# Kernel optimization log

Measured on AMD Instinct MI355X. Metric: run time of the kernel, lower is better.

## Reference

```python
import math
import jax, jax.numpy as jnp
import numpy as np

DIM = 256
B, S = 4, 4096

def setup_inputs() -> dict:
    key = jax.random.key(0)
    k1, k2, k3, k4 = jax.random.split(key, 4)
    x = jax.random.normal(k1, (B, S, DIM), dtype=jnp.float32)
    W = jax.random.normal(k2, (3 * DIM, DIM), dtype=jnp.float32) * 0.02
    b = jax.random.normal(k3, (3 * DIM,), dtype=jnp.float32) * 0.02
    attention_mask = jax.random.randint(k4, (B, 1, S), 0, 2, dtype=jnp.int32)
    return {"x": x, "W": W, "b": b, "attention_mask": attention_mask}

def reference(x, W, b, attention_mask):
    # qkv projection: Linear(dim, 3*dim) -> x @ W^T + b
    qkv = jnp.einsum("bsd,ed->bse", x, W) + b  # [B,S,3*DIM]
    q, k, v = jnp.split(qkv, 3, axis=-1)
    # NOTE: module computes q @ v^T (not q @ k^T) -- faithful to source
    scores = jnp.einsum("bqd,bkd->bqk", q, v) / math.sqrt(DIM)  # [B,S,S]
    scores = jnp.where(attention_mask == 0, -jnp.inf, scores)
    attn = jax.nn.softmax(scores, axis=-1)
    # dropout in eval mode -> identity
    out = jnp.einsum("bqk,bkd->bqd", attn, v)  # [B,S,DIM]
    return out
```

## Files before the change

kernel.cpp:

```cpp
#include <hip/hip_runtime.h>
#include <hip/hip_bf16.h>

#define DIMC 256
#define NB 4
#define NS 4096
#define KT 64
#define VS_ELEMS (KT * DIMC)

typedef __attribute__((ext_vector_type(4))) float f32x4;
typedef __attribute__((ext_vector_type(8))) short bf16x8;

__device__ __forceinline__ ushort f2bf(float f) {
  __hip_bfloat16 h = __float2bfloat16(f);
  return *reinterpret_cast<ushort*>(&h);
}
__device__ __forceinline__ float bf2f(ushort h) {
  uint u = ((uint)h) << 16;
  float f;
  __builtin_memcpy(&f, &u, 4);
  return f;
}

__device__ __forceinline__ void gload16(const ushort* g, ushort* l) {
  __builtin_amdgcn_global_load_lds(
      (const __attribute__((address_space(1))) unsigned int*)g,
      (__attribute__((address_space(3))) unsigned int*)l,
      16, 0, 0);
}

__global__ __launch_bounds__(256) void prep_kernel(
    const float* __restrict__ W, const int* __restrict__ mask,
    ushort* __restrict__ Whl, uint* __restrict__ pm32)
{
  if (blockIdx.x < 512) {
    const int col = blockIdx.x;
    const int k = threadIdx.x;
    const int srcrow = (col < 256) ? col : (col + 256);
    float f = W[(size_t)srcrow * 256 + k];
    ushort h = f2bf(f);
    Whl[(size_t)col * 256 + k] = h;
    Whl[131072 + (size_t)col * 256 + k] = f2bf(f - bf2f(h));
  } else {
    int t = (blockIdx.x - 512) * 256 + threadIdx.x;
    int b = t >> 7;
    int kt = (t >> 1) & 63;
    int kh = t & 1;
    const int* mrow = mask + b * NS + kt * 64 + kh * 32;
    uint wd = 0;
    for (int g = 0; g < 4; ++g)
      for (int ntl = 0; ntl < 2; ++ntl)
        for (int r = 0; r < 4; ++r)
          if (mrow[ntl * 16 + 4 * g + r] != 0) wd |= 1u << (8 * g + ntl * 4 + r);
    pm32[t] = wd;
  }
}

__global__ __launch_bounds__(256) void qv_proj_kernel(
    const float* __restrict__ x, const ushort* __restrict__ Whl,
    const float* __restrict__ bias,
    ushort* __restrict__ qb, ushort* __restrict__ vb, ushort* __restrict__ vtb)
{
  const int tid  = threadIdx.x;
  const int w    = tid >> 6;
  const int lane = tid & 63;
  const int l15  = lane & 15;
  const int g    = (lane >> 4) & 3;
  const int r0   = blockIdx.x << 6;
  const int colbase = w << 7;

  __shared__ ushort olds[64 * 520];

  f32x4 acc[4][8];
  #pragma unroll
  for (int rt = 0; rt < 4; ++rt)
    #pragma unroll
    for (int ct = 0; ct < 8; ++ct) { acc[rt][ct].x=0.f; acc[rt][ct].y=0.f; acc[rt][ct].z=0.f; acc[rt][ct].w=0.f; }

  #pragma unroll 1
  for (int st = 0; st < 8; ++st) {
    bf16x8 xh[4], xl[4];
    #pragma unroll
    for (int rt = 0; rt < 4; ++rt) {
      const float* p = x + (size_t)(r0 + rt * 16 + l15) * DIMC + st * 32 + g * 8;
      float4 f0 = *(const float4*)p;
      float4 f1 = *(const float4*)(p + 4);
      union { bf16x8 v; ushort u[8]; } uh, ul;
      #pragma unroll
      for (int e = 0; e < 8; ++e) {
        float fe = (e < 4) ? ((const float*)&f0)[e] : ((const float*)&f1)[e - 4];
        ushort h = f2bf(fe);
        uh.u[e] = h;
        ul.u[e] = f2bf(fe - bf2f(h));
      }
      xh[rt] = uh.v;
      xl[rt] = ul.v;
    }
    #pragma unroll
    for (int ct = 0; ct < 8; ++ct) {
      const ushort* wp = Whl + (size_t)(colbase + ct * 16 + l15) * 256 + st * 32 + g * 8;
      bf16x8 wh = *(const bf16x8*)wp;
      bf16x8 wl = *(const bf16x8*)(wp + 131072);
      #pragma unroll
      for (int rt = 0; rt < 4; ++rt) {
        acc[rt][ct] = __builtin_amdgcn_mfma_f32_16x16x32_bf16(xh[rt], wh, acc[rt][ct], 0, 0, 0);
        acc[rt][ct] = __builtin_amdgcn_mfma_f32_16x16x32_bf16(xl[rt], wh, acc[rt][ct], 0, 0, 0);
        acc[rt][ct] = __builtin_amdgcn_mfma_f32_16x16x32_bf16(xh[rt], wl, acc[rt][ct], 0, 0, 0);
      }
    }
  }

  const float qscale = (colbase < 256) ? 0.0625f : 1.0f;
  #pragma unroll
  for (int ct = 0; ct < 8; ++ct) {
    const int col = colbase + ct * 16 + l15;
    const float bv = bias[(col < 256) ? col : (col + 256)];
    #pragma unroll
    for (int rt = 0; rt < 4; ++rt) {
      #pragma unroll
      for (int r = 0; r < 4; ++r)
        olds[(rt * 16 + 4 * g + r) * 520 + col] = f2bf((acc[rt][ct][r] + bv) * qscale);
    }
  }
  __syncthreads();

  #pragma unroll
  for (int i = 0; i < 16; ++i) {
    int task = tid + i * 256;
    int row = task >> 6, ch = task & 63;
    uint4 d = *(const uint4*)&olds[row * 520 + ch * 8];
    if (ch < 32) *(uint4*)&qb[(size_t)(r0 + row) * DIMC + ch * 8] = d;
    else         *(uint4*)&vb[(size_t)(r0 + row) * DIMC + (ch - 32) * 8] = d;
  }
  const int bbp = r0 >> 12;
  const int s0  = r0 & (NS - 1);
  const int vcol = tid;
  #pragma unroll
  for (int o = 0; o < 8; ++o) {
    union { uint4 v; ushort u[8]; } pk;
    #pragma unroll
    for (int j = 0; j < 8; ++j)
      pk.u[j] = olds[(o * 8 + j) * 520 + 256 + vcol];
    *(uint4*)&vtb[((size_t)(bbp * DIMC + vcol)) * NS + s0 + o * 8] = pk.v;
  }
}

__global__ __launch_bounds__(512, 1) void attn_kernel(
    const ushort* __restrict__ qb, const ushort* __restrict__ vb,
    const ushort* __restrict__ vtb, const uint* __restrict__ pm32,
    float* __restrict__ outA, float* __restrict__ opB,
    float* __restrict__ mlA, float* __restrict__ mlB)
{
  const int tid  = threadIdx.x;
  const int w    = tid >> 6;
  const int lane = tid & 63;
  const int l15  = lane & 15;
  const int g    = (lane >> 4) & 3;
  const int kh   = w & 1;
  const int pq   = w >> 1;

  const int s     = blockIdx.x & 1;
  const int qb128 = blockIdx.x >> 1;
  const int qrow0 = qb128 << 7;
  const int bb    = qrow0 >> 12;
  const int koff  = s << 11;

  float* opart = s ? opB : outA;
  float* mlp   = s ? mlB : mlA;

  extern __shared__ __align__(16) char smem[];
  uint*   pmlds = (uint*)smem;
  ushort* vs0  = (ushort*)(smem + 1024);
  ushort* vs1  = vs0 + VS_ELEMS;
  ushort* vt0  = vs1 + VS_ELEMS;
  ushort* vt1  = vt0 + VS_ELEMS;
  ushort* psb  = vt1 + VS_ELEMS;

  bf16x8 qreg[2][8];
  #pragma unroll
  for (int qt = 0; qt < 2; ++qt) {
    const int qrow = qrow0 + (pq << 5) + (qt << 4) + l15;
    #pragma unroll
    for (int st = 0; st < 8; ++st)
      qreg[qt][st] = *(const bf16x8*)&qb[(size_t)qrow * DIMC + ((st * 4 + g) << 3)];
  }

  if (tid < 128) pmlds[tid] = pm32[(bb << 7) + tid];

  auto stage_vs = [&](int kt, ushort* vsN) {
    const ushort* vbase = vb + ((size_t)(bb * NS + koff + kt * KT)) * DIMC;
    #pragma unroll
    for (int i = 0; i < 4; ++i) {
      int rr0 = (w << 3) + (i << 1);
      int row = rr0 + (lane >> 5);
      int cs  = lane & 31;
      gload16(vbase + row * DIMC + ((cs ^ (row & 7)) << 3), vsN + (rr0 << 8));
    }
  };
  auto stage_vt = [&](int kt, ushort* vtN) {
    #pragma unroll
    for (int i = 0; i < 4; ++i) {
      int d0 = i << 6;
      int dim = (d0 + lane) ^ ((w & 3) << 1);
      gload16(vtb + ((size_t)(bb * DIMC + dim)) * NS + koff + kt * KT + (w << 3),
              vtN + ((w << 8) + d0) * 8);
    }
  };

  stage_vs(0, vs0);
  __syncthreads();

  f32x4 acc_o[2][8];
  #pragma unroll
  for (int qt = 0; qt < 2; ++qt)
    #pragma unroll
    for (int nt = 0; nt < 8; ++nt) { acc_o[qt][nt].x=0.f; acc_o[qt][nt].y=0.f; acc_o[qt][nt].z=0.f; acc_o[qt][nt].w=0.f; }
  float l_s[2] = {0.f, 0.f};

  ushort* psw = psb + pq * (32 * 72);

  #pragma unroll 1
  for (int t = 0; t < 32; ++t) {
    ushort* vsQ = (t & 1) ? vs1 : vs0;
    ushort* vsS = (t & 1) ? vs0 : vs1;
    ushort* vtS = (t & 1) ? vt1 : vt0;
    ushort* vtP = (t & 1) ? vt0 : vt1;

    if (t + 1 < 32) stage_vs(t + 1, vsS);
    stage_vt(t, vtS);

    f32x4 sacc[2][2];
    #pragma unroll
    for (int qt = 0; qt < 2; ++qt) {
      sacc[qt][0].x=0.f; sacc[qt][0].y=0.f; sacc[qt][0].z=0.f; sacc[qt][0].w=0.f;
      sacc[qt][1] = sacc[qt][0];
    }
    __builtin_amdgcn_s_setprio(1);
    #pragma unroll
    for (int st = 0; st < 8; ++st) {
      const int key0 = (kh << 5) + l15;
      bf16x8 af0 = *(const bf16x8*)&vsQ[(key0 * 32 + ((st * 4 + g) ^ (key0 & 7))) * 8];
      const int key1 = key0 + 16;
      bf16x8 af1 = *(const bf16x8*)&vsQ[(key1 * 32 + ((st * 4 + g) ^ (key1 & 7))) * 8];
      #pragma unroll
      for (int qt = 0; qt < 2; ++qt) {
        sacc[qt][0] = __builtin_amdgcn_mfma_f32_16x16x32_bf16(af0, qreg[qt][st], sacc[qt][0], 0, 0, 0);
        sacc[qt][1] = __builtin_amdgcn_mfma_f32_16x16x32_bf16(af1, qreg[qt][st], sacc[qt][1], 0, 0, 0);
      }
    }
    __builtin_amdgcn_s_setprio(0);

    if (t > 0) {
      bf16x8 pa[2][2];
      #pragma unroll
      for (int qt = 0; qt < 2; ++qt)
        #pragma unroll
        for (int ks2 = 0; ks2 < 2; ++ks2)
          pa[qt][ks2] = *(const bf16x8*)&psw[((qt << 4) + l15) * 72 + (ks2 << 5) + (g << 3)];
      __builtin_amdgcn_s_setprio(1);
      #pragma unroll
      for (int ntl = 0; ntl < 8; ++ntl) {
        const int d = ((kh << 3) + ntl) * 16 + l15;
        #pragma unroll
        for (int ks2 = 0; ks2 < 2; ++ks2) {
          const int kc = (ks2 << 2) + g;
          bf16x8 vf = *(const bf16x8*)&vtP[((kc << 8) + (d ^ ((kc & 3) << 1))) * 8];
          acc_o[0][ntl] = __builtin_amdgcn_mfma_f32_16x16x32_bf16(vf, pa[0][ks2], acc_o[0][ntl], 0, 0, 0);
          acc_o[1][ntl] = __builtin_amdgcn_mfma_f32_16x16x32_bf16(vf, pa[1][ks2], acc_o[1][ntl], 0, 0, 0);
        }
      }
      __builtin_amdgcn_s_setprio(0);
    }

    const int ktg = (s << 5) + t;
    uint mybits = (pmlds[(ktg << 1) + kh] >> (g << 3)) & 0xffu;
    float pv[2][8];
    #pragma unroll
    for (int qt = 0; qt < 2; ++qt) {
      #pragma unroll
      for (int ntl = 0; ntl < 2; ++ntl)
        #pragma unroll
        for (int r = 0; r < 4; ++r) {
          float vv = (mybits & (1u << (ntl * 4 + r))) ? sacc[qt][ntl][r] : -1e30f;
          pv[qt][ntl * 4 + r] = __expf(vv);
        }
      float rs = ((pv[qt][0] + pv[qt][1]) + (pv[qt][2] + pv[qt][3])) +
                 ((pv[qt][4] + pv[qt][5]) + (pv[qt][6] + pv[qt][7]));
      rs += __shfl_xor(rs, 16);
      rs += __shfl_xor(rs, 32);
      l_s[qt] += rs;
    }

    asm volatile("s_waitcnt lgkmcnt(0)" ::: "memory");
    __builtin_amdgcn_sched_barrier(0);
    __builtin_amdgcn_s_barrier();
    __builtin_amdgcn_sched_barrier(0);

    #pragma unroll
    for (int qt = 0; qt < 2; ++qt) {
      #pragma unroll
      for (int ntl = 0; ntl < 2; ++ntl) {
        uint2 pk;
        pk.x = (uint)f2bf(pv[qt][ntl*4+0]) | ((uint)f2bf(pv[qt][ntl*4+1]) << 16);
        pk.y = (uint)f2bf(pv[qt][ntl*4+2]) | ((uint)f2bf(pv[qt][ntl*4+3]) << 16);
        *(uint2*)&psw[((qt << 4) + l15) * 72 + (kh << 5) + ntl * 16 + 4 * g] = pk;
      }
    }

    if (t + 1 < 32)
      asm volatile("s_waitcnt vmcnt(8) lgkmcnt(0)" ::: "memory");
    else
      asm volatile("s_waitcnt vmcnt(4) lgkmcnt(0)" ::: "memory");
    __builtin_amdgcn_sched_barrier(0);
    __builtin_amdgcn_s_barrier();
    __builtin_amdgcn_sched_barrier(0);
  }

  asm volatile("s_waitcnt vmcnt(0)" ::: "memory");
  __builtin_amdgcn_sched_barrier(0);
  __builtin_amdgcn_s_barrier();
  __builtin_amdgcn_sched_barrier(0);
  {
    ushort* vtP = vt1;
    bf16x8 pa[2][2];
    #pragma unroll
    for (int qt = 0; qt < 2; ++qt)
      #pragma unroll
      for (int ks2 = 0; ks2 < 2; ++ks2)
        pa[qt][ks2] = *(const bf16x8*)&psw[((qt << 4) + l15) * 72 + (ks2 << 5) + (g << 3)];
    __builtin_amdgcn_s_setprio(1);
    #pragma unroll
    for (int ntl = 0; ntl < 8; ++ntl) {
      const int d = ((kh << 3) + ntl) * 16 + l15;
      #pragma unroll
      for (int ks2 = 0; ks2 < 2; ++ks2) {
        const int kc = (ks2 << 2) + g;
        bf16x8 vf = *(const bf16x8*)&vtP[((kc << 8) + (d ^ ((kc & 3) << 1))) * 8];
        acc_o[0][ntl] = __builtin_amdgcn_mfma_f32_16x16x32_bf16(vf, pa[0][ks2], acc_o[0][ntl], 0, 0, 0);
        acc_o[1][ntl] = __builtin_amdgcn_mfma_f32_16x16x32_bf16(vf, pa[1][ks2], acc_o[1][ntl], 0, 0, 0);
      }
    }
    __builtin_amdgcn_s_setprio(0);
  }

  #pragma unroll
  for (int qt = 0; qt < 2; ++qt) {
    const int qrow = qrow0 + (pq << 5) + (qt << 4) + l15;
    const size_t obase = (size_t)qrow * DIMC + 4 * g;
    #pragma unroll
    for (int ntl = 0; ntl < 8; ++ntl) {
      f32x4 o = acc_o[qt][ntl];
      *(float4*)&opart[obase + ((kh << 3) + ntl) * 16] = *(float4*)&o;
    }
    if (g == 0) mlp[(size_t)qrow * 2 + kh] = l_s[qt];
  }
}

__global__ __launch_bounds__(256) void merge_kernel(
    float* __restrict__ outA, const float* __restrict__ opB,
    const float* __restrict__ mlA, const float* __restrict__ mlB)
{
  int id = blockIdx.x * 256 + threadIdx.x;
  int row = id >> 6;
  int c = (id & 63) << 2;
  float lT = (mlA[(size_t)row * 2] + mlA[(size_t)row * 2 + 1]) +
             (mlB[(size_t)row * 2] + mlB[(size_t)row * 2 + 1]);
  float inv = 1.f / lT;
  size_t o = (size_t)row * DIMC + c;
  float4 a = *(const float4*)&outA[o];
  float4 b = *(const float4*)&opB[o];
  float4 r;
  r.x = (a.x + b.x) * inv;
  r.y = (a.y + b.y) * inv;
  r.z = (a.z + b.z) * inv;
  r.w = (a.w + b.w) * inv;
  *(float4*)&outA[o] = r;
}

extern "C" void kernel_launch(void* const* d_in, const int* in_sizes, int n_in,
                              void* d_out, int out_size, void* d_ws, size_t ws_size,
                              hipStream_t stream) {
  const float* x    = (const float*)d_in[0];
  const float* W    = (const float*)d_in[1];
  const float* bias = (const float*)d_in[2];
  const int*   mask = (const int*)d_in[3];
  float* out = (float*)d_out;

  const size_t n = (size_t)NB * NS * DIMC;
  ushort* qb  = (ushort*)d_ws;
  ushort* vb  = qb + n;
  ushort* vtb = vb + n;
  uint* pm32 = (uint*)(vtb + n);
  ushort* Whl = (ushort*)(pm32 + 512);
  float* opB = (float*)(Whl + 262144);
  float* mlA = opB + n;
  float* mlB = mlA + 2 * (NB * NS);

  prep_kernel<<<514, 256, 0, stream>>>(W, mask, Whl, pm32);
  qv_proj_kernel<<<(NB * NS) / 64, 256, 0, stream>>>(x, Whl, bias, qb, vb, vtb);

  const int smem_bytes = 1024 + 4 * VS_ELEMS * 2 + 4 * 32 * 72 * 2;
  attn_kernel<<<256, 512, smem_bytes, stream>>>(qb, vb, vtb, pm32, out, opB, mlA, mlB);
  merge_kernel<<<(NB * NS * DIMC / 4) / 256, 256, 0, stream>>>(out, opB, mlA, mlB);
}
```

Baseline: 147.8 us.

## Precompute bf16 hi/lo split of x in prep kernel; widen projection blocks

After: 147.4 us (median of 3 runs). No clear change (-0.3%).

```diff
diff --git a/kernel.cpp b/kernel.cpp
--- a/kernel.cpp
+++ b/kernel.cpp
@@ -30,18 +30,21 @@
 
 __global__ __launch_bounds__(256) void prep_kernel(
     const float* __restrict__ W, const int* __restrict__ mask,
-    ushort* __restrict__ Whl, uint* __restrict__ pm32)
+    const float* __restrict__ x,
+    ushort* __restrict__ Whl, uint* __restrict__ pm32,
+    ushort* __restrict__ xhb, ushort* __restrict__ xlb)
 {
-  if (blockIdx.x < 512) {
-    const int col = blockIdx.x;
+  const int bid = blockIdx.x;
+  if (bid < 512) {
+    const int col = bid;
     const int k = threadIdx.x;
     const int srcrow = (col < 256) ? col : (col + 256);
     float f = W[(size_t)srcrow * 256 + k];
     ushort h = f2bf(f);
     Whl[(size_t)col * 256 + k] = h;
     Whl[131072 + (size_t)col * 256 + k] = f2bf(f - bf2f(h));
-  } else {
-    int t = (blockIdx.x - 512) * 256 + threadIdx.x;
+  } else if (bid < 514) {
+    int t = (bid - 512) * 256 + threadIdx.x;
     int b = t >> 7;
     int kt = (t >> 1) & 63;
     int kh = t & 1;
@@ -52,12 +55,26 @@
         for (int r = 0; r < 4; ++r)
           if (mrow[ntl * 16 + 4 * g + r] != 0) wd |= 1u << (8 * g + ntl * 4 + r);
     pm32[t] = wd;
-  }
-}
-
-__global__ __launch_bounds__(256) void qv_proj_kernel(
-    const float* __restrict__ x, const ushort* __restrict__ Whl,
-    const float* __restrict__ bias,
+  } else {
+    size_t idx = ((size_t)(bid - 514) * 256 + threadIdx.x) * 8;
+    float4 f0 = *(const float4*)&x[idx];
+    float4 f1 = *(const float4*)&x[idx + 4];
+    union { uint4 v; ushort u[8]; } ph, pl;
+    #pragma unroll
+    for (int e = 0; e < 8; ++e) {
+      float fe = (e < 4) ? ((const float*)&f0)[e] : ((const float*)&f1)[e - 4];
+      ushort h = f2bf(fe);
+      ph.u[e] = h;
+      pl.u[e] = f2bf(fe - bf2f(h));
+    }
+    *(uint4*)&xhb[idx] = ph.v;
+    *(uint4*)&xlb[idx] = pl.v;
+  }
+}
+
+__global__ __launch_bounds__(512) void qv_proj_kernel(
+    const ushort* __restrict__ xhb, const ushort* __restrict__ xlb,
+    const ushort* __restrict__ Whl, const float* __restrict__ bias,
     ushort* __restrict__ qb, ushort* __restrict__ vb, ushort* __restrict__ vtb)
 {
   const int tid  = threadIdx.x;
@@ -66,37 +83,27 @@
   const int l15  = lane & 15;
   const int g    = (lane >> 4) & 3;
   const int r0   = blockIdx.x << 6;
-  const int colbase = w << 7;
+  const int colbase = w << 6;
 
   __shared__ ushort olds[64 * 520];
 
-  f32x4 acc[4][8];
+  f32x4 acc[4][4];
   #pragma unroll
   for (int rt = 0; rt < 4; ++rt)
     #pragma unroll
-    for (int ct = 0; ct < 8; ++ct) { acc[rt][ct].x=0.f; acc[rt][ct].y=0.f; acc[rt][ct].z=0.f; acc[rt][ct].w=0.f; }
+    for (int ct = 0; ct < 4; ++ct) { acc[rt][ct].x=0.f; acc[rt][ct].y=0.f; acc[rt][ct].z=0.f; acc[rt][ct].w=0.f; }
 
   #pragma unroll 1
   for (int st = 0; st < 8; ++st) {
     bf16x8 xh[4], xl[4];
     #pragma unroll
     for (int rt = 0; rt < 4; ++rt) {
-      const float* p = x + (size_t)(r0 + rt * 16 + l15) * DIMC + st * 32 + g * 8;
-      float4 f0 = *(const float4*)p;
-      float4 f1 = *(const float4*)(p + 4);
-      union { bf16x8 v; ushort u[8]; } uh, ul;
-      #pragma unroll
-      for (int e = 0; e < 8; ++e) {
-        float fe = (e < 4) ? ((const float*)&f0)[e] : ((const float*)&f1)[e - 4];
-        ushort h = f2bf(fe);
-        uh.u[e] = h;
-        ul.u[e] = f2bf(fe - bf2f(h));
-      }
-      xh[rt] = uh.v;
-      xl[rt] = ul.v;
-    }
-    #pragma unroll
-    for (int ct = 0; ct < 8; ++ct) {
+      const size_t off = (size_t)(r0 + rt * 16 + l15) * DIMC + st * 32 + g * 8;
+      xh[rt] = *(const bf16x8*)&xhb[off];
+      xl[rt] = *(const bf16x8*)&xlb[off];
+    }
+    #pragma unroll
+    for (int ct = 0; ct < 4; ++ct) {
       const ushort* wp = Whl + (size_t)(colbase + ct * 16 + l15) * 256 + st * 32 + g * 8;
       bf16x8 wh = *(const bf16x8*)wp;
       bf16x8 wl = *(const bf16x8*)(wp + 131072);
@@ -111,7 +118,7 @@
 
   const float qscale = (colbase < 256) ? 0.0625f : 1.0f;
   #pragma unroll
-  for (int ct = 0; ct < 8; ++ct) {
+  for (int ct = 0; ct < 4; ++ct) {
     const int col = colbase + ct * 16 + l15;
     const float bv = bias[(col < 256) ? col : (col + 256)];
     #pragma unroll
@@ -124,8 +131,8 @@
   __syncthreads();
 
   #pragma unroll
-  for (int i = 0; i < 16; ++i) {
-    int task = tid + i * 256;
+  for (int i = 0; i < 8; ++i) {
+    int task = tid + i * 512;
     int row = task >> 6, ch = task & 63;
     uint4 d = *(const uint4*)&olds[row * 520 + ch * 8];
     if (ch < 32) *(uint4*)&qb[(size_t)(r0 + row) * DIMC + ch * 8] = d;
@@ -133,9 +140,11 @@
   }
   const int bbp = r0 >> 12;
   const int s0  = r0 & (NS - 1);
-  const int vcol = tid;
-  #pragma unroll
-  for (int o = 0; o < 8; ++o) {
+  const int vcol = tid & 255;
+  const int ohalf = (tid >> 8) * 4;
+  #pragma unroll
+  for (int oo = 0; oo < 4; ++oo) {
+    int o = ohalf + oo;
     union { uint4 v; ushort u[8]; } pk;
     #pragma unroll
     for (int j = 0; j < 8; ++j)
@@ -394,9 +403,11 @@
   float* opB = (float*)(Whl + 262144);
   float* mlA = opB + n;
   float* mlB = mlA + 2 * (NB * NS);
-
-  prep_kernel<<<514, 256, 0, stream>>>(W, mask, Whl, pm32);
-  qv_proj_kernel<<<(NB * NS) / 64, 256, 0, stream>>>(x, Whl, bias, qb, vb, vtb);
+  ushort* xhb = (ushort*)opB;
+  ushort* xlb = xhb + n;
+
+  prep_kernel<<<2562, 256, 0, stream>>>(W, mask, x, Whl, pm32, xhb, xlb);
+  qv_proj_kernel<<<(NB * NS) / 64, 512, 0, stream>>>(xhb, xlb, Whl, bias, qb, vb, vtb);
 
   const int smem_bytes = 1024 + 4 * VS_ELEMS * 2 + 4 * 32 * 72 * 2;
   attn_kernel<<<256, 512, smem_bytes, stream>>>(qb, vb, vtb, pm32, out, opB, mlA, mlB);
```
